# Performance work log

Measured on AMD Instinct MI355X. Metric: run time of the kernel, lower is better.

## Reference

```python
import jax, jax.numpy as jnp
import numpy as np

B, S, H, N_IN, N_OUT = 8, 2048, 16, 128, 128


def setup_inputs() -> dict:
    key = jax.random.key(0)
    k1, k2 = jax.random.split(key)
    inputs = jax.random.normal(k1, (B, S, H, N_IN), dtype=jnp.float32)
    # stacked ParameterList: W[h] is the (n_out, n_in) block for head h
    W = jax.random.normal(k2, (H, N_OUT, N_IN), dtype=jnp.float32) * 0.02
    return {"inputs": inputs, "W": W}


def reference(inputs, W):
    # Block-diagonal projection: each head h gets its own (n_out, n_in) matrix.
    # Equivalent to the torch loop of per-head GEMVs, expressed as one einsum.
    # inputs: [b, s, h, i], W: [h, o, i] -> out: [b, s, h, o]
    return jnp.einsum("bshi,hoi->bsho", inputs, W)
```

## Files before the change

### kernel.cpp

```cpp
#include <hip/hip_runtime.h>
#include <hip/hip_bf16.h>

typedef __attribute__((ext_vector_type(4))) float  f4;
typedef __attribute__((ext_vector_type(8))) short  short8;
typedef __attribute__((ext_vector_type(4))) float  f32x4;

static constexpr int NHEAD = 16;
static constexpr int NIN   = 128;
static constexpr int NOUT  = 128;
static constexpr int NROWS = 8 * 2048;
static constexpr int RSTR  = NHEAD * NIN;
static constexpr int ROWS_PER_BLOCK = 128;
static constexpr int BLOCKS_X = NROWS / ROWS_PER_BLOCK;

static __device__ inline unsigned short f2bfu(float f) {
  union { __hip_bfloat16 h; unsigned short u; } v;
  v.h = __float2bfloat16(f);
  return v.u;
}

static __device__ inline short8 cvt8(f4 a, f4 b) {
  short8 r;
  r[0] = (short)f2bfu(a[0]); r[1] = (short)f2bfu(a[1]);
  r[2] = (short)f2bfu(a[2]); r[3] = (short)f2bfu(a[3]);
  r[4] = (short)f2bfu(b[0]); r[5] = (short)f2bfu(b[1]);
  r[6] = (short)f2bfu(b[2]); r[7] = (short)f2bfu(b[3]);
  return r;
}

__global__ __launch_bounds__(512)
void bdp_kernel(const float* __restrict__ X, const float* __restrict__ W,
                float* __restrict__ O) {
  __shared__ short8 wtile[32][64];

  const int head = blockIdx.y;
  const int tid  = (int)threadIdx.x;
  const int lane = tid & 63;
  const int wid  = tid >> 6;
  const int lr   = lane & 15;
  const int lq   = lane >> 4;

  const int row0 = (int)blockIdx.x * ROWS_PER_BLOCK + wid * 16;
  const float* xr = X + (size_t)(row0 + lr) * RSTR + head * NIN;

  f4 xa[4], xb[4];
  #pragma unroll
  for (int kk = 0; kk < 4; ++kk) {
    const int koff = kk * 32 + lq * 8;
    xa[kk] = *reinterpret_cast<const f4*>(xr + koff);
    xb[kk] = *reinterpret_cast<const f4*>(xr + koff + 4);
  }

  const float* Wh = W + (size_t)head * NOUT * NIN;
  #pragma unroll
  for (int it = 0; it < 4; ++it) {
    const int frag = wid * 4 + it;
    const int n  = frag >> 2;
    const int kk = frag & 3;
    const float* src = Wh + (n * 16 + lr) * NIN + kk * 32 + lq * 8;
    f4 a = *reinterpret_cast<const f4*>(src);
    f4 b = *reinterpret_cast<const f4*>(src + 4);
    wtile[frag][lane] = cvt8(a, b);
  }
  __syncthreads();

  short8 xv[4];
  #pragma unroll
  for (int kk = 0; kk < 4; ++kk) xv[kk] = cvt8(xa[kk], xb[kk]);

  f32x4 acc[8];
  #pragma unroll
  for (int n = 0; n < 8; ++n) acc[n] = (f32x4){0.f, 0.f, 0.f, 0.f};

  #pragma unroll
  for (int kk = 0; kk < 4; ++kk) {
    #pragma unroll
    for (int n = 0; n < 8; ++n) {
      acc[n] = __builtin_amdgcn_mfma_f32_16x16x32_bf16(
          wtile[n * 4 + kk][lane], xv[kk], acc[n], 0, 0, 0);
    }
  }

  float* dst = O + (size_t)(row0 + lr) * RSTR + head * NOUT;
  #pragma unroll
  for (int n = 0; n < 8; ++n) {
    __builtin_nontemporal_store(acc[n], reinterpret_cast<f4*>(dst + n * 16 + lq * 4));
  }
}

extern "C" void kernel_launch(void* const* d_in, const int* in_sizes, int n_in,
                              void* d_out, int out_size, void* d_ws, size_t ws_size,
                              hipStream_t stream) {
  const float* X = (const float*)d_in[0];
  const float* W = (const float*)d_in[1];
  float* O = (float*)d_out;
  dim3 grid(BLOCKS_X, NHEAD);
  bdp_kernel<<<grid, dim3(512), 0, stream>>>(X, W, O);
}
```

Measured before the change: 61.00 us.

## Keep W fragments in registers and loop each block over row steps

```diff
diff --git a/kernel.cpp b/kernel.cpp
--- a/kernel.cpp
+++ b/kernel.cpp
@@ -10,8 +10,11 @@
 static constexpr int NOUT  = 128;
 static constexpr int NROWS = 8 * 2048;
 static constexpr int RSTR  = NHEAD * NIN;
-static constexpr int ROWS_PER_BLOCK = 128;
+static constexpr int ROWS_PER_STEP  = 32;
+static constexpr int STEPS          = 8;
+static constexpr int ROWS_PER_BLOCK = ROWS_PER_STEP * STEPS;
 static constexpr int BLOCKS_X = NROWS / ROWS_PER_BLOCK;
+
 
 static __device__ inline unsigned short f2bfu(float f) {
   union { __hip_bfloat16 h; unsigned short u; } v;
@@ -28,63 +31,52 @@
   return r;
 }
 
-__global__ __launch_bounds__(512)
+__global__ __launch_bounds__(512, 4)
 void bdp_kernel(const float* __restrict__ X, const float* __restrict__ W,
                 float* __restrict__ O) {
-  __shared__ short8 wtile[32][64];
-
   const int head = blockIdx.y;
   const int tid  = (int)threadIdx.x;
   const int lane = tid & 63;
   const int wid  = tid >> 6;
   const int lr   = lane & 15;
   const int lq   = lane >> 4;
+  const int rg   = wid & 1;
+  const int nh   = wid >> 1;
 
-  const int row0 = (int)blockIdx.x * ROWS_PER_BLOCK + wid * 16;
-  const float* xr = X + (size_t)(row0 + lr) * RSTR + head * NIN;
-
-  f4 xa[4], xb[4];
+  const float* Wh = W + (size_t)head * NOUT * NIN;
+  short8 wf0[4], wf1[4];
   #pragma unroll
   for (int kk = 0; kk < 4; ++kk) {
-    const int koff = kk * 32 + lq * 8;
-    xa[kk] = *reinterpret_cast<const f4*>(xr + koff);
-    xb[kk] = *reinterpret_cast<const f4*>(xr + koff + 4);
+    const float* s0 = Wh + ((2 * nh + 0) * 16 + lr) * NIN + kk * 32 + lq * 8;
+    const float* s1 = Wh + ((2 * nh + 1) * 16 + lr) * NIN + kk * 32 + lq * 8;
+    wf0[kk] = cvt8(*reinterpret_cast<const f4*>(s0),
+                   *reinterpret_cast<const f4*>(s0 + 4));
+    wf1[kk] = cvt8(*reinterpret_cast<const f4*>(s1),
+                   *reinterpret_cast<const f4*>(s1 + 4));
   }
 
-  const float* Wh = W + (size_t)head * NOUT * NIN;
-  #pragma unroll
-  for (int it = 0; it < 4; ++it) {
-    const int frag = wid * 4 + it;
-    const int n  = frag >> 2;
-    const int kk = frag & 3;
-    const float* src = Wh + (n * 16 + lr) * NIN + kk * 32 + lq * 8;
-    f4 a = *reinterpret_cast<const f4*>(src);
-    f4 b = *reinterpret_cast<const f4*>(src + 4);
-    wtile[frag][lane] = cvt8(a, b);
-  }
-  __syncthreads();
+  const int rowbase = (int)blockIdx.x * ROWS_PER_BLOCK + rg * 16;
+  const float* xr = X + (size_t)(rowbase + lr) * RSTR + head * NIN;
+  float* orow     = O + (size_t)(rowbase + lr) * RSTR + head * NOUT;
 
-  short8 xv[4];
-  #pragma unroll
-  for (int kk = 0; kk < 4; ++kk) xv[kk] = cvt8(xa[kk], xb[kk]);
+  for (int t = 0; t < STEPS; ++t) {
+    const float* xt = xr + (size_t)t * ROWS_PER_STEP * RSTR;
 
-  f32x4 acc[8];
-  #pragma unroll
-  for (int n = 0; n < 8; ++n) acc[n] = (f32x4){0.f, 0.f, 0.f, 0.f};
+    f32x4 acc0 = (f32x4){0.f, 0.f, 0.f, 0.f};
+    f32x4 acc1 = (f32x4){0.f, 0.f, 0.f, 0.f};
+    #pragma unroll
+    for (int kk = 0; kk < 4; ++kk) {
+      const int koff = kk * 32 + lq * 8;
+      f4 a = *reinterpret_cast<const f4*>(xt + koff);
+      f4 b = *reinterpret_cast<const f4*>(xt + koff + 4);
+      short8 xv = cvt8(a, b);
+      acc0 = __builtin_amdgcn_mfma_f32_16x16x32_bf16(wf0[kk], xv, acc0, 0, 0, 0);
+      acc1 = __builtin_amdgcn_mfma_f32_16x16x32_bf16(wf1[kk], xv, acc1, 0, 0, 0);
+    }
 
-  #pragma unroll
-  for (int kk = 0; kk < 4; ++kk) {
-    #pragma unroll
-    for (int n = 0; n < 8; ++n) {
-      acc[n] = __builtin_amdgcn_mfma_f32_16x16x32_bf16(
-          wtile[n * 4 + kk][lane], xv[kk], acc[n], 0, 0, 0);
-    }
-  }
-
-  float* dst = O + (size_t)(row0 + lr) * RSTR + head * NOUT;
-  #pragma unroll
-  for (int n = 0; n < 8; ++n) {
-    __builtin_nontemporal_store(acc[n], reinterpret_cast<f4*>(dst + n * 16 + lq * 4));
+    float* dst = orow + (size_t)t * ROWS_PER_STEP * RSTR;
+    *reinterpret_cast<f4*>(dst + (2 * nh + 0) * 16 + lq * 4) = acc0;
+    *reinterpret_cast<f4*>(dst + (2 * nh + 1) * 16 + lq * 4) = acc1;
   }
 }
 
```

Measured after the change: 98.09 us. 60.8% more time.
